# Performance work log

Hardware: AMD Instinct MI355X
Metric: run time of the kernel (lower is better)

The kernel has to match this reference:

```python
import jax, jax.numpy as jnp
import numpy as np

EPS = 1e-5  # torch InstanceNorm3d default eps


def setup_inputs() -> dict:
    key = jax.random.key(0)
    kx, kw, kb = jax.random.split(key, 3)
    # x: (B, C_in, T, D, H, W)
    x = jax.random.normal(kx, (1, 4, 8, 96, 96, 96), dtype=jnp.float32)
    # 4D hypercube conv kernel: (C_out, C_in, kT, kD, kH, kW)
    w = jax.random.normal(kw, (8, 4, 3, 3, 3, 3), dtype=jnp.float32) * 0.05
    b = jax.random.normal(kb, (8,), dtype=jnp.float32) * 0.05
    return {"x": x, "w": w, "b": b}


def reference(x, w, b):
    # Per-time-slice InstanceNorm3d (affine=False): normalizing each t-slice
    # over (D,H,W) per (b,c) is identical to normalizing over spatial dims
    # per (b,c,t) in one fused pass (the torch loop + stack is just this).
    mean = jnp.mean(x, axis=(3, 4, 5), keepdims=True)
    var = jnp.var(x, axis=(3, 4, 5), keepdims=True)  # biased, as in torch
    xn = (x - mean) * jax.lax.rsqrt(var + EPS)
    # ReLU activation
    xa = jax.nn.relu(xn)
    # True 4D convolution (T,D,H,W spatial), padding=1 everywhere, stride 1.
    # This equals the repo's Conv4d (sum of per-temporal-offset Conv3d's).
    out = jax.lax.conv_general_dilated(
        xa, w,
        window_strides=(1, 1, 1, 1),
        padding=[(1, 1)] * 4,
        dimension_numbers=("NCTDHW", "OITDHW", "NCTDHW"),
    )
    return out + b.reshape(1, -1, 1, 1, 1, 1)
```

## Files before the change

kernel.cpp:

```cpp
#include <hip/hip_runtime.h>

#define CI 4
#define CO 8
#define TT 8
#define S 96
#define S2 (S*S)
#define SLICE (S*S*S)
#define NSLICE (CI*TT)
#define EPS 1e-5f
#define WTOT (CO*CI*81)
#define WS_WT_OFF 64


__global__ __launch_bounds__(256) void stats_partial(
        const float* __restrict__ x, float* __restrict__ ws) {
    const int slice = blockIdx.y;
    const float4* p = reinterpret_cast<const float4*>(x + (size_t)slice * SLICE);
    const int n4 = SLICE / 4;
    float s = 0.f, ss = 0.f;
    for (int i = blockIdx.x * blockDim.x + threadIdx.x; i < n4;
         i += gridDim.x * blockDim.x) {
        float4 v = p[i];
        s  += v.x + v.y + v.z + v.w;
        ss += v.x*v.x + v.y*v.y + v.z*v.z + v.w*v.w;
    }
    #pragma unroll
    for (int off = 32; off > 0; off >>= 1) {
        s  += __shfl_down(s, off);
        ss += __shfl_down(ss, off);
    }
    __shared__ float ls[4], lss[4];
    const int lane = threadIdx.x & 63, wid = threadIdx.x >> 6;
    if (lane == 0) { ls[wid] = s; lss[wid] = ss; }
    __syncthreads();
    if (threadIdx.x == 0) {
        float ts  = ls[0] + ls[1] + ls[2] + ls[3];
        float tss = lss[0] + lss[1] + lss[2] + lss[3];
        atomicAdd(&ws[slice], ts);
        atomicAdd(&ws[NSLICE + slice], tss);
    }
}

__global__ void wtranspose(const float* __restrict__ w, float* __restrict__ wt) {
    int i = blockIdx.x * blockDim.x + threadIdx.x;
    if (i >= WTOT) return;
    int kw = i % 3; int r = i / 3;
    int co = r % CO; r /= CO;
    int kh = r % 3;  r /= 3;
    int kd = r % 3;  r /= 3;
    int kt = r % 3;  r /= 3;
    int ci = r;
    wt[i] = w[((((co * CI + ci) * 3 + kt) * 3 + kd) * 3 + kh) * 3 + kw];
}

template <bool TW>
__global__ __launch_bounds__(192, 3) void conv4d_fused(
        const float* __restrict__ x, const float* __restrict__ wsrc,
        const float* __restrict__ bias, const float* __restrict__ ws,
        float* __restrict__ out) {
    const int lane = threadIdx.x;
    const int ty   = threadIdx.y;
    const int w0   = lane << 2;
    const int d    = blockIdx.x;
    const int h0   = (blockIdx.y * 8 + ty) * 2;
    const int t    = blockIdx.z;

    float acc[2][CO][4];
    #pragma unroll
    for (int p = 0; p < 2; p++)
        #pragma unroll
        for (int co = 0; co < CO; co++)
            #pragma unroll
            for (int j = 0; j < 4; j++) acc[p][co][j] = 0.f;

    const bool wlb = (lane > 0), wrb = (lane < 23);
    const int  om1 = wlb ? -1 : 0;
    const int  op4 = wrb ?  4 : 3;
    const float fwl = wlb ? 1.f : 0.f, fwr = wrb ? 1.f : 0.f;
    const float inv_n = 1.f / (float)SLICE;

    const int dm1 = d > 0 ? d - 1 : 0;
    const int dp1 = d < S - 1 ? d + 1 : S - 1;
    const float md0 = d > 0 ? 1.f : 0.f;
    const float md2 = d < S - 1 ? 1.f : 0.f;
    float mr0, mr1, mr2, mr3;
    int o0, o1, o2, o3;
    {
        const int hh0 = h0 - 1, hh3 = h0 + 2;
        mr0 = ((unsigned)hh0 < S) ? 1.f : 0.f;
        mr1 = 1.f; mr2 = 1.f;
        mr3 = ((unsigned)hh3 < S) ? 1.f : 0.f;
        const int hc0 = hh0 < 0 ? 0 : hh0;
        const int hc3 = hh3 > S - 1 ? S - 1 : hh3;
        o0 = hc0 * S + w0; o1 = h0 * S + w0;
        o2 = (h0 + 1) * S + w0; o3 = hc3 * S + w0;
    }

    const int ktlo = (t == 0) ? 1 : 0;
    const int kthi = (t == TT - 1) ? 1 : 2;
    const int nkt  = kthi - ktlo + 1;
    const int niter = CI * nkt;

    #define DECL_BUF(N) \
        float4 f##N##0, f##N##1, f##N##2, f##N##3; \
        float e##N##00, e##N##01, e##N##02, e##N##03; \
        float e##N##10, e##N##11, e##N##12, e##N##13;
    DECL_BUF(A) DECL_BUF(B) DECL_BUF(C)

    #define LOAD_BUF(N, XP) do { \
        const float* _r0 = (XP) + o0; const float* _r1 = (XP) + o1; \
        const float* _r2 = (XP) + o2; const float* _r3 = (XP) + o3; \
        f##N##0 = *reinterpret_cast<const float4*>(_r0); \
        f##N##1 = *reinterpret_cast<const float4*>(_r1); \
        f##N##2 = *reinterpret_cast<const float4*>(_r2); \
        f##N##3 = *reinterpret_cast<const float4*>(_r3); \
        e##N##00 = _r0[om1]; e##N##01 = _r1[om1]; \
        e##N##02 = _r2[om1]; e##N##03 = _r3[om1]; \
        e##N##10 = _r0[op4]; e##N##11 = _r1[op4]; \
        e##N##12 = _r2[op4]; e##N##13 = _r3[op4]; \
    } while (0)

    #define NORM_ROW(N, R, MR, MD) do { \
        const float m_ = (MR) * (MD); \
        const float rs = rstd * m_, nm = nmr * m_; \
        nn[R][0] = fwl * fmaxf(fmaf(e##N##0##R, rs, nm), 0.f); \
        nn[R][1] =       fmaxf(fmaf(f##N##R.x,  rs, nm), 0.f); \
        nn[R][2] =       fmaxf(fmaf(f##N##R.y,  rs, nm), 0.f); \
        nn[R][3] =       fmaxf(fmaf(f##N##R.z,  rs, nm), 0.f); \
        nn[R][4] =       fmaxf(fmaf(f##N##R.w,  rs, nm), 0.f); \
        nn[R][5] = fwr * fmaxf(fmaf(e##N##1##R, rs, nm), 0.f); \
    } while (0)

    #define COMPUTE_BUF(N, WP, MD) do { \
        float nn[4][6]; \
        NORM_ROW(N, 0, mr0, MD); NORM_ROW(N, 1, mr1, MD); \
        NORM_ROW(N, 2, mr2, MD); NORM_ROW(N, 3, mr3, MD); \
        _Pragma("unroll") \
        for (int kh = 0; kh < 3; kh++) { \
            _Pragma("unroll") \
            for (int q = 0; q < 3; q++) { \
                _Pragma("unroll") \
                for (int co = 0; co < CO; co++) { \
                    const float k_ = TW ? (WP)[kh * 24 + co * 3 + q] \
                                        : (WP)[co * (CI * 81) + kh * 3 + q]; \
                    _Pragma("unroll") \
                    for (int j = 0; j < 4; j++) { \
                        acc[0][co][j] = fmaf(nn[kh][j + q],     k_, acc[0][co][j]); \
                        acc[1][co][j] = fmaf(nn[kh + 1][j + q], k_, acc[1][co][j]); \
                    } \
                } \
            } \
        } \
    } while (0)

    int ci = 0, kt = ktlo;
    int sl = ci * TT + (t + kt - 1);
    const float* xs = x + (size_t)sl * SLICE;
    const float* xp2;
    float rstd, nmr;
    {
        const float mean = ws[sl] * inv_n;
        const float var  = ws[NSLICE + sl] * inv_n - mean * mean;
        rstd = rsqrtf(var + EPS);
        nmr  = -mean * rstd;
    }
    const float* wp = TW ? (wsrc + (ci * 3 + kt) * 216)
                         : (wsrc + ci * 81 + kt * 27);
    xp2 = xs + (size_t)dp1 * S2;
    LOAD_BUF(A, xs + (size_t)dm1 * S2);
    LOAD_BUF(B, xs + (size_t)d   * S2);

    for (int it = 0; it < niter; it++) {
        LOAD_BUF(C, xp2);

        COMPUTE_BUF(A, wp, md0);

        int kt_n = kt, ci_n = ci;
        if (it + 1 < niter) {
            kt_n = kt + 1;
            if (kt_n > kthi) { kt_n = ktlo; ci_n = ci + 1; }
        }
        const int sl_n = ci_n * TT + (t + kt_n - 1);
        const float* xs_n = x + (size_t)sl_n * SLICE;
        const float mean_n = ws[sl_n] * inv_n;
        const float var_n  = ws[NSLICE + sl_n] * inv_n - mean_n * mean_n;
        const float rstd_n = rsqrtf(var_n + EPS);
        const float nmr_n  = -mean_n * rstd_n;
        const float* wp_n = TW ? (wsrc + (ci_n * 3 + kt_n) * 216)
                               : (wsrc + ci_n * 81 + kt_n * 27);

        LOAD_BUF(A, xs_n + (size_t)dm1 * S2);

        COMPUTE_BUF(B, TW ? wp + 72 : wp + 9, 1.f);

        LOAD_BUF(B, xs_n + (size_t)d * S2);

        COMPUTE_BUF(C, TW ? wp + 144 : wp + 18, md2);

        rstd = rstd_n; nmr = nmr_n; wp = wp_n;
        xp2 = xs_n + (size_t)dp1 * S2;
        ci = ci_n; kt = kt_n;
    }

    #undef DECL_BUF
    #undef LOAD_BUF
    #undef NORM_ROW
    #undef COMPUTE_BUF

    #pragma unroll
    for (int p = 0; p < 2; p++) {
        const size_t obase = (((size_t)t * S + d) * S + (h0 + p)) * S + w0;
        #pragma unroll
        for (int co = 0; co < CO; co++) {
            const float bb = bias[co];
            float4 o;
            o.x = acc[p][co][0] + bb;
            o.y = acc[p][co][1] + bb;
            o.z = acc[p][co][2] + bb;
            o.w = acc[p][co][3] + bb;
            *reinterpret_cast<float4*>(out + (size_t)co * ((size_t)TT * SLICE) + obase) = o;
        }
    }
}

extern "C" void kernel_launch(void* const* d_in, const int* in_sizes, int n_in,
                              void* d_out, int out_size, void* d_ws, size_t ws_size,
                              hipStream_t stream) {
    const float* x   = (const float*)d_in[0];
    const float* w   = (const float*)d_in[1];
    const float* b   = (const float*)d_in[2];
    float* out = (float*)d_out;
    float* ws  = (float*)d_ws;

    const bool tw = ws_size >= (size_t)(WS_WT_OFF + WTOT) * sizeof(float);

    hipMemsetAsync(ws, 0, 2 * NSLICE * sizeof(float), stream);
    stats_partial<<<dim3(64, NSLICE), 256, 0, stream>>>(x, ws);
    if (tw) {
        wtranspose<<<(WTOT + 255) / 256, 256, 0, stream>>>(w, ws + WS_WT_OFF);
        conv4d_fused<true><<<dim3(S, S / 16, TT), dim3(24, 8, 1), 0, stream>>>(
                x, ws + WS_WT_OFF, b, ws, out);
    } else {
        conv4d_fused<false><<<dim3(S, S / 16, TT), dim3(24, 8, 1), 0, stream>>>(
                x, w, b, ws, out);
    }
}
```

Measured before the change: 648.7 us.

## Fuse weight transpose into stats kernel, remap blocks per XCD, prefetch weights

The separate weight-transpose kernel is folded into the stats kernel, which saves one launch. The conv grid becomes 1D and is remapped so each XCD (blockIdx mod 8) handles a contiguous range of depth slices, aiming for better L2 reuse of neighbouring input planes. In the transposed-weight path, weights are loaded as float4 groups into registers one phase ahead of their use, software-pipelining weight loads against the FMAs. The extra live weight registers could raise register pressure and lower occupancy under launch_bounds(192,3).

```diff
diff --git a/kernel.cpp b/kernel.cpp
--- a/kernel.cpp
+++ b/kernel.cpp
@@ -13,7 +13,8 @@
 
 
 __global__ __launch_bounds__(256) void stats_partial(
-        const float* __restrict__ x, float* __restrict__ ws) {
+        const float* __restrict__ x, float* __restrict__ ws,
+        const float* __restrict__ w, float* __restrict__ wt) {
     const int slice = blockIdx.y;
     const float4* p = reinterpret_cast<const float4*>(x + (size_t)slice * SLICE);
     const int n4 = SLICE / 4;
@@ -39,18 +40,18 @@
         atomicAdd(&ws[slice], ts);
         atomicAdd(&ws[NSLICE + slice], tss);
     }
-}
-
-__global__ void wtranspose(const float* __restrict__ w, float* __restrict__ wt) {
-    int i = blockIdx.x * blockDim.x + threadIdx.x;
-    if (i >= WTOT) return;
-    int kw = i % 3; int r = i / 3;
-    int co = r % CO; r /= CO;
-    int kh = r % 3;  r /= 3;
-    int kd = r % 3;  r /= 3;
-    int kt = r % 3;  r /= 3;
-    int ci = r;
-    wt[i] = w[((((co * CI + ci) * 3 + kt) * 3 + kd) * 3 + kh) * 3 + kw];
+    if (wt != nullptr && blockIdx.y == 0) {
+        for (int i = blockIdx.x * blockDim.x + threadIdx.x; i < WTOT;
+             i += 64 * 256) {
+            int kw = i % 3; int r = i / 3;
+            int co = r % CO; r /= CO;
+            int kh = r % 3;  r /= 3;
+            int kd = r % 3;  r /= 3;
+            int kt = r % 3;  r /= 3;
+            int ci = r;
+            wt[i] = w[((((co * CI + ci) * 3 + kt) * 3 + kd) * 3 + kh) * 3 + kw];
+        }
+    }
 }
 
 template <bool TW>
@@ -58,12 +59,18 @@
         const float* __restrict__ x, const float* __restrict__ wsrc,
         const float* __restrict__ bias, const float* __restrict__ ws,
         float* __restrict__ out) {
+    const int o   = blockIdx.x;
+    const int xcd = o & 7;
+    const int ii  = o >> 3;
+    const int d   = xcd * 12 + ii / 48;
+    const int rr  = ii % 48;
+    const int t   = rr / 6;
+    const int hb  = rr % 6;
+
     const int lane = threadIdx.x;
     const int ty   = threadIdx.y;
     const int w0   = lane << 2;
-    const int d    = blockIdx.x;
-    const int h0   = (blockIdx.y * 8 + ty) * 2;
-    const int t    = blockIdx.z;
+    const int h0   = (hb * 8 + ty) * 2;
 
     float acc[2][CO][4];
     #pragma unroll
@@ -120,33 +127,61 @@
         e##N##12 = _r2[op4]; e##N##13 = _r3[op4]; \
     } while (0)
 
-    #define NORM_ROW(N, R, MR, MD) do { \
+    #define NORM_ROW(NN, N, R, MR, MD) do { \
         const float m_ = (MR) * (MD); \
         const float rs = rstd * m_, nm = nmr * m_; \
-        nn[R][0] = fwl * fmaxf(fmaf(e##N##0##R, rs, nm), 0.f); \
-        nn[R][1] =       fmaxf(fmaf(f##N##R.x,  rs, nm), 0.f); \
-        nn[R][2] =       fmaxf(fmaf(f##N##R.y,  rs, nm), 0.f); \
-        nn[R][3] =       fmaxf(fmaf(f##N##R.z,  rs, nm), 0.f); \
-        nn[R][4] =       fmaxf(fmaf(f##N##R.w,  rs, nm), 0.f); \
-        nn[R][5] = fwr * fmaxf(fmaf(e##N##1##R, rs, nm), 0.f); \
-    } while (0)
-
-    #define COMPUTE_BUF(N, WP, MD) do { \
-        float nn[4][6]; \
-        NORM_ROW(N, 0, mr0, MD); NORM_ROW(N, 1, mr1, MD); \
-        NORM_ROW(N, 2, mr2, MD); NORM_ROW(N, 3, mr3, MD); \
+        NN[R][0] = fwl * fmaxf(fmaf(e##N##0##R, rs, nm), 0.f); \
+        NN[R][1] =       fmaxf(fmaf(f##N##R.x,  rs, nm), 0.f); \
+        NN[R][2] =       fmaxf(fmaf(f##N##R.y,  rs, nm), 0.f); \
+        NN[R][3] =       fmaxf(fmaf(f##N##R.z,  rs, nm), 0.f); \
+        NN[R][4] =       fmaxf(fmaf(f##N##R.w,  rs, nm), 0.f); \
+        NN[R][5] = fwr * fmaxf(fmaf(e##N##1##R, rs, nm), 0.f); \
+    } while (0)
+
+    #define NORM4(NN, N, MD) do { \
+        NORM_ROW(NN, N, 0, mr0, MD); NORM_ROW(NN, N, 1, mr1, MD); \
+        NORM_ROW(NN, N, 2, mr2, MD); NORM_ROW(NN, N, 3, mr3, MD); \
+    } while (0)
+
+    #define WLOAD(DST, PTR) do { \
+        const float4* _w4 = reinterpret_cast<const float4*>(PTR); \
+        float4 _a = _w4[0], _b = _w4[1], _c = _w4[2]; \
+        float4 _d4 = _w4[3], _e = _w4[4], _f = _w4[5]; \
+        DST[0]=_a.x;   DST[1]=_a.y;   DST[2]=_a.z;   DST[3]=_a.w;  \
+        DST[4]=_b.x;   DST[5]=_b.y;   DST[6]=_b.z;   DST[7]=_b.w;  \
+        DST[8]=_c.x;   DST[9]=_c.y;   DST[10]=_c.z;  DST[11]=_c.w; \
+        DST[12]=_d4.x; DST[13]=_d4.y; DST[14]=_d4.z; DST[15]=_d4.w;\
+        DST[16]=_e.x;  DST[17]=_e.y;  DST[18]=_e.z;  DST[19]=_e.w; \
+        DST[20]=_f.x;  DST[21]=_f.y;  DST[22]=_f.z;  DST[23]=_f.w; \
+    } while (0)
+
+    #define PHASE(NN, KH, WARR) do { \
+        _Pragma("unroll") \
+        for (int q = 0; q < 3; q++) { \
+            _Pragma("unroll") \
+            for (int co = 0; co < CO; co++) { \
+                const float k_ = WARR[co * 3 + q]; \
+                _Pragma("unroll") \
+                for (int j = 0; j < 4; j++) { \
+                    acc[0][co][j] = fmaf(NN[KH][j + q],     k_, acc[0][co][j]); \
+                    acc[1][co][j] = fmaf(NN[KH + 1][j + q], k_, acc[1][co][j]); \
+                } \
+            } \
+        } \
+    } while (0)
+
+    #define COMPUTE_OLD(NN, WP) do { \
         _Pragma("unroll") \
         for (int kh = 0; kh < 3; kh++) { \
             _Pragma("unroll") \
             for (int q = 0; q < 3; q++) { \
                 _Pragma("unroll") \
                 for (int co = 0; co < CO; co++) { \
-                    const float k_ = TW ? (WP)[kh * 24 + co * 3 + q] \
-                                        : (WP)[co * (CI * 81) + kh * 3 + q]; \
+                    const float k_ = (WP)[co * (CI * 81) + kh * 3 + q]; \
                     _Pragma("unroll") \
                     for (int j = 0; j < 4; j++) { \
-                        acc[0][co][j] = fmaf(nn[kh][j + q],     k_, acc[0][co][j]); \
-                        acc[1][co][j] = fmaf(nn[kh + 1][j + q], k_, acc[1][co][j]); \
+                        acc[0][co][j] = fmaf(NN[kh][j + q],     k_, acc[0][co][j]); \
+                        acc[1][co][j] = fmaf(NN[kh + 1][j + q], k_, acc[1][co][j]); \
                     } \
                 } \
             } \
@@ -171,10 +206,6 @@
     LOAD_BUF(B, xs + (size_t)d   * S2);
 
     for (int it = 0; it < niter; it++) {
-        LOAD_BUF(C, xp2);
-
-        COMPUTE_BUF(A, wp, md0);
-
         int kt_n = kt, ci_n = ci;
         if (it + 1 < niter) {
             kt_n = kt + 1;
@@ -189,13 +220,39 @@
         const float* wp_n = TW ? (wsrc + (ci_n * 3 + kt_n) * 216)
                                : (wsrc + ci_n * 81 + kt_n * 27);
 
-        LOAD_BUF(A, xs_n + (size_t)dm1 * S2);
-
-        COMPUTE_BUF(B, TW ? wp + 72 : wp + 9, 1.f);
-
-        LOAD_BUF(B, xs_n + (size_t)d * S2);
-
-        COMPUTE_BUF(C, TW ? wp + 144 : wp + 18, md2);
+        if constexpr (TW) {
+            float wg0[24]; WLOAD(wg0, wp);
+            LOAD_BUF(C, xp2);
+
+            float nnA[4][6]; NORM4(nnA, A, md0);
+            float wg1[24]; WLOAD(wg1, wp + 24);  PHASE(nnA, 0, wg0);
+            float wg2[24]; WLOAD(wg2, wp + 48);  PHASE(nnA, 1, wg1);
+            float wg3[24]; WLOAD(wg3, wp + 72);  PHASE(nnA, 2, wg2);
+
+            LOAD_BUF(A, xs_n + (size_t)dm1 * S2);
+
+            float nnB[4][6]; NORM4(nnB, B, 1.f);
+            float wg4[24]; WLOAD(wg4, wp + 96);  PHASE(nnB, 0, wg3);
+            float wg5[24]; WLOAD(wg5, wp + 120); PHASE(nnB, 1, wg4);
+            float wg6[24]; WLOAD(wg6, wp + 144); PHASE(nnB, 2, wg5);
+
+            LOAD_BUF(B, xs_n + (size_t)d * S2);
+
+            float nnC[4][6]; NORM4(nnC, C, md2);
+            float wg7[24]; WLOAD(wg7, wp + 168); PHASE(nnC, 0, wg6);
+            float wg8[24]; WLOAD(wg8, wp + 192); PHASE(nnC, 1, wg7);
+                                                 PHASE(nnC, 2, wg8);
+        } else {
+            LOAD_BUF(C, xp2);
+            float nnA[4][6]; NORM4(nnA, A, md0);
+            COMPUTE_OLD(nnA, wp);
+            LOAD_BUF(A, xs_n + (size_t)dm1 * S2);
+            float nnB[4][6]; NORM4(nnB, B, 1.f);
+            COMPUTE_OLD(nnB, wp + 9);
+            LOAD_BUF(B, xs_n + (size_t)d * S2);
+            float nnC[4][6]; NORM4(nnC, C, md2);
+            COMPUTE_OLD(nnC, wp + 18);
+        }
 
         rstd = rstd_n; nmr = nmr_n; wp = wp_n;
         xp2 = xs_n + (size_t)dp1 * S2;
@@ -205,7 +262,10 @@
     #undef DECL_BUF
     #undef LOAD_BUF
     #undef NORM_ROW
-    #undef COMPUTE_BUF
+    #undef NORM4
+    #undef WLOAD
+    #undef PHASE
+    #undef COMPUTE_OLD
 
     #pragma unroll
     for (int p = 0; p < 2; p++) {
@@ -213,12 +273,12 @@
         #pragma unroll
         for (int co = 0; co < CO; co++) {
             const float bb = bias[co];
-            float4 o;
-            o.x = acc[p][co][0] + bb;
-            o.y = acc[p][co][1] + bb;
-            o.z = acc[p][co][2] + bb;
-            o.w = acc[p][co][3] + bb;
-            *reinterpret_cast<float4*>(out + (size_t)co * ((size_t)TT * SLICE) + obase) = o;
+            float4 ov;
+            ov.x = acc[p][co][0] + bb;
+            ov.y = acc[p][co][1] + bb;
+            ov.z = acc[p][co][2] + bb;
+            ov.w = acc[p][co][3] + bb;
+            *reinterpret_cast<float4*>(out + (size_t)co * ((size_t)TT * SLICE) + obase) = ov;
         }
     }
 }
@@ -233,15 +293,15 @@
     float* ws  = (float*)d_ws;
 
     const bool tw = ws_size >= (size_t)(WS_WT_OFF + WTOT) * sizeof(float);
+    float* wt = tw ? (ws + WS_WT_OFF) : nullptr;
 
     hipMemsetAsync(ws, 0, 2 * NSLICE * sizeof(float), stream);
-    stats_partial<<<dim3(64, NSLICE), 256, 0, stream>>>(x, ws);
+    stats_partial<<<dim3(64, NSLICE), 256, 0, stream>>>(x, ws, w, wt);
     if (tw) {
-        wtranspose<<<(WTOT + 255) / 256, 256, 0, stream>>>(w, ws + WS_WT_OFF);
-        conv4d_fused<true><<<dim3(S, S / 16, TT), dim3(24, 8, 1), 0, stream>>>(
+        conv4d_fused<true><<<S * (S / 16) * TT, dim3(24, 8, 1), 0, stream>>>(
                 x, ws + WS_WT_OFF, b, ws, out);
     } else {
-        conv4d_fused<false><<<dim3(S, S / 16, TT), dim3(24, 8, 1), 0, stream>>>(
+        conv4d_fused<false><<<S * (S / 16) * TT, dim3(24, 8, 1), 0, stream>>>(
                 x, w, b, ws, out);
     }
 }
```

After: 661.4 us. Within noise of the previous version (+1.9%).
